# Kernel optimization log

Measured on AMD Instinct MI355X. Metric: run time of the kernel, lower is better.

The kernel has to match this reference:

```python
import jax, jax.numpy as jnp
import numpy as np

POOL_SCALES = (1, 3, 6, 8)
CHANNELS = 256
BN_EPS = 1e-5


def _pool_matrix(in_size, out_size):
    # Row i averages input slots [floor(i*in/out), ceil((i+1)*in/out)) -- matches AdaptiveAvgPool2d.
    P = np.zeros((out_size, in_size), np.float32)
    for i in range(out_size):
        s = (i * in_size) // out_size
        e = -((-(i + 1) * in_size) // out_size)
        P[i, s:e] = 1.0 / (e - s)
    return jnp.asarray(P)


def _bn(x, g, b, m, v):
    # inference-mode BatchNorm2d on NCHW
    inv = g * jax.lax.rsqrt(v + BN_EPS)
    return x * inv[None, :, None, None] + (b - m * inv)[None, :, None, None]


def _conv1x1(x, w):
    # 1x1 conv == channel matmul: w [Cout, Cin], x [B, Cin, H, W]
    return jnp.einsum('oc,bchw->bohw', w, x)


def _ppm_concat(x):
    # x: [B, C, H, W] -> [B, C, sum(s*s)]
    B, C, H, W = x.shape
    outs = []
    for s in POOL_SCALES:
        Ph = _pool_matrix(H, s)
        Pw = _pool_matrix(W, s)
        pooled = jnp.einsum('ih,jw,bchw->bcij', Ph, Pw, x)
        outs.append(pooled.reshape(B, C, -1))
    return jnp.concatenate(outs, axis=2)


def setup_inputs() -> dict:
    key = jax.random.key(0)
    ks = jax.random.split(key, 24)
    B, Cl, Ch, Cmid, Cout, H, W = 8, 1024, 2048, 256, 2048, 64, 64
    return {
        'low_feats': jax.random.normal(ks[0], (B, Cl, H, W), jnp.float32),
        'high_feats': jax.random.normal(ks[1], (B, Ch, H, W), jnp.float32),
        'q_w': jax.random.normal(ks[2], (Cmid, Ch), jnp.float32) * 0.02,
        'q_g': jax.random.uniform(ks[3], (Cmid,), jnp.float32, 0.5, 1.5),
        'q_b': jax.random.normal(ks[4], (Cmid,), jnp.float32) * 0.1,
        'q_m': jax.random.normal(ks[5], (Cmid,), jnp.float32) * 0.1,
        'q_v': jax.random.uniform(ks[6], (Cmid,), jnp.float32, 0.5, 1.5),
        'k_w': jax.random.normal(ks[7], (Cmid, Cl), jnp.float32) * 0.02,
        'k_g': jax.random.uniform(ks[8], (Cmid,), jnp.float32, 0.5, 1.5),
        'k_b': jax.random.normal(ks[9], (Cmid,), jnp.float32) * 0.1,
        'k_m': jax.random.normal(ks[10], (Cmid,), jnp.float32) * 0.1,
        'k_v': jax.random.uniform(ks[11], (Cmid,), jnp.float32, 0.5, 1.5),
        'v_w': jax.random.normal(ks[12], (Cmid, Cl), jnp.float32) * 0.02,
        'v_b': jax.random.normal(ks[13], (Cmid,), jnp.float32) * 0.02,
        'o_w': jax.random.normal(ks[14], (Cout, Cmid), jnp.float32) * 0.02,
        'o_b': jax.random.normal(ks[15], (Cout,), jnp.float32) * 0.02,
        'bn_w': jax.random.normal(ks[16], (Cout, Cout + Ch), jnp.float32) * 0.02,
        'bn_g': jax.random.uniform(ks[17], (Cout,), jnp.float32, 0.5, 1.5),
        'bn_b': jax.random.normal(ks[18], (Cout,), jnp.float32) * 0.1,
        'bn_m': jax.random.normal(ks[19], (Cout,), jnp.float32) * 0.1,
        'bn_v': jax.random.uniform(ks[20], (Cout,), jnp.float32, 0.5, 1.5),
    }


def reference(low_feats, high_feats, q_w, q_g, q_b, q_m, q_v,
              k_w, k_g, k_b, k_m, k_v, v_w, v_b, o_w, o_b,
              bn_w, bn_g, bn_b, bn_m, bn_v):
    B, _, H, W = high_feats.shape
    # query: ConvModule (1x1 conv, BN, ReLU) on high-level feats; query_scale=1 -> no downsample
    q = jax.nn.relu(_bn(_conv1x1(high_feats, q_w), q_g, q_b, q_m, q_v))
    q = q.reshape(B, CHANNELS, H * W).transpose(0, 2, 1)  # [B, N, C]
    # key: ConvModule then pyramid-pooled; value: plain 1x1 conv then pyramid-pooled
    k = jax.nn.relu(_bn(_conv1x1(low_feats, k_w), k_g, k_b, k_m, k_v))
    k = _ppm_concat(k)  # [B, C, M]
    v = _conv1x1(low_feats, v_w) + v_b[None, :, None, None]
    v = _ppm_concat(v).transpose(0, 2, 1)  # [B, M, C]
    # matmul-normalized attention with pooled K/V (M = 110, tiny)
    sim = jnp.einsum('bnc,bcm->bnm', q, k) * (CHANNELS ** -0.5)
    sim = jax.nn.softmax(sim, axis=-1)
    ctx = jnp.einsum('bnm,bmc->bnc', sim, v)  # [B, N, C]
    ctx = ctx.transpose(0, 2, 1).reshape(B, CHANNELS, H, W)
    # out projection: plain 1x1 conv with bias
    ctx = _conv1x1(ctx, o_w) + o_b[None, :, None, None]  # [B, Cout, H, W]
    # single stage (query_scales=(1,)), stack+sum is identity
    # bottleneck: 1x1 conv (no bias) + BN, no activation
    fused = jnp.concatenate([ctx, high_feats], axis=1)
    out = _bn(_conv1x1(fused, bn_w), bn_g, bn_b, bn_m, bn_v)
    return out
```

## Files before the change

### kernel.cpp

```cpp
#include <hip/hip_runtime.h>
#include <hip/hip_bf16.h>

typedef unsigned int u32;
typedef unsigned short u16;
typedef short s16x8 __attribute__((ext_vector_type(8)));
typedef float f32x4 __attribute__((ext_vector_type(4)));
typedef u16 u16x4 __attribute__((ext_vector_type(4)));

__device__ __forceinline__ u16 f2b(float x) {
  u32 u = __float_as_uint(x);
  return (u16)((u + 0x7fffu + ((u >> 16) & 1u)) >> 16);
}
__device__ __forceinline__ float b2f(u16 x) { return __uint_as_float(((u32)x) << 16); }

__device__ __forceinline__ void gload16(const void* g, void* l) {
  __builtin_amdgcn_global_load_lds((const __attribute__((address_space(1))) u32*)g,
                                   (__attribute__((address_space(3))) u32*)l, 16, 0, 0);
}

template <int OUT_BF16>
__global__ __launch_bounds__(512, 2) void gemm256(
    const u16* __restrict__ A, long long sA, int lda,
    const u16* __restrict__ B1, long long sB1, int K1,
    const u16* __restrict__ B2, long long sB2, int K2,
    void* __restrict__ Cv, long long sC, int ldc,
    const float* __restrict__ bias, int bias_mode,
    int relu_limit, float alpha) {
  const int K = K1 + K2, nt = K >> 5;
  const int b = blockIdx.z, tm = blockIdx.x, tn = blockIdx.y;
  const u16* Ab = A + (size_t)b * sA + (size_t)tm * 256 * lda;
  const u16* B1b = B1 + (size_t)b * sB1 + (size_t)tn * 256 * K1;
  const u16* B2b = B2 ? (B2 + (size_t)b * sB2 + (size_t)tn * 256 * K2) : (const u16*)0;

  __shared__ u16 lds[32768];

  const int tt = threadIdx.x, w = tt >> 6, l = tt & 63;
  const int wr = w >> 2, wc = w & 3;

  int sx[2], sdst[2];
#pragma unroll
  for (int i = 0; i < 2; ++i) {
    const int lin = (i * 512 + tt) << 4;
    sx[i] = lin ^ (((lin >> 7) & 7) << 4);
    sdst[i] = (i * 512 + w * 64) << 3;
  }

  auto stage = [&](int kt) {
    const int buf = (kt & 1) << 14;
    const int kk = kt << 5;
#pragma unroll
    for (int i = 0; i < 2; ++i) {
      const int x = sx[i];
      gload16(Ab + (size_t)(x >> 6) * lda + kk + ((x & 63) >> 1), &lds[buf + sdst[i]]);
    }
    const u16* Bb; int ld, kloc;
    if (kk < K1) { Bb = B1b; ld = K1; kloc = kk; }
    else         { Bb = B2b; ld = K2; kloc = kk - K1; }
#pragma unroll
    for (int i = 0; i < 2; ++i) {
      const int x = sx[i];
      gload16(Bb + (size_t)(x >> 6) * ld + kloc + ((x & 63) >> 1), &lds[buf + 8192 + sdst[i]]);
    }
  };

  stage(0);
  stage(1);

  f32x4 acc[8][4] = {};
  const int lr = l & 15, lk16 = (l >> 4) << 4;

  for (int t = 0; t < nt; ++t) {
    const int buf = (t & 1) << 14;
    if (t == nt - 1) asm volatile("s_waitcnt vmcnt(0)" ::: "memory");
    else             asm volatile("s_waitcnt vmcnt(4)" ::: "memory");
    __builtin_amdgcn_s_barrier();

    const char* Abuf = (const char*)&lds[buf];
    const char* Bbuf = (const char*)&lds[buf + 8192];
    s16x8 bfr[4], af[8];
#pragma unroll
    for (int j = 0; j < 4; ++j) {
      const int lin = ((wc * 64 + j * 16 + lr) << 6) | lk16;
      bfr[j] = *reinterpret_cast<const s16x8*>(Bbuf + (lin ^ (((lin >> 7) & 7) << 4)));
    }
#pragma unroll
    for (int m = 0; m < 8; ++m) {
      const int lin = ((wr * 128 + m * 16 + lr) << 6) | lk16;
      af[m] = *reinterpret_cast<const s16x8*>(Abuf + (lin ^ (((lin >> 7) & 7) << 4)));
    }
    __builtin_amdgcn_s_setprio(1);
#pragma unroll
    for (int m = 0; m < 4; ++m)
#pragma unroll
      for (int j = 0; j < 4; ++j)
        acc[m][j] = __builtin_amdgcn_mfma_f32_16x16x32_bf16(af[m], bfr[j], acc[m][j], 0, 0, 0);
    __builtin_amdgcn_s_setprio(0);

    asm volatile("s_waitcnt lgkmcnt(0)" ::: "memory");
    __builtin_amdgcn_s_barrier();
    if (t + 2 < nt) stage(t + 2);

    __builtin_amdgcn_s_setprio(1);
#pragma unroll
    for (int m = 4; m < 8; ++m)
#pragma unroll
      for (int j = 0; j < 4; ++j)
        acc[m][j] = __builtin_amdgcn_mfma_f32_16x16x32_bf16(af[m], bfr[j], acc[m][j], 0, 0, 0);
    __builtin_amdgcn_s_setprio(0);
  }

  const int li = (l >> 4) * 4;
#pragma unroll
  for (int m = 0; m < 8; ++m) {
    const int row = tm * 256 + wr * 128 + m * 16 + li;
#pragma unroll
    for (int j = 0; j < 4; ++j) {
      const int col = tn * 256 + wc * 64 + j * 16 + lr;
      const float bc = (bias_mode == 1) ? bias[col] : 0.f;
#pragma unroll
      for (int i = 0; i < 4; ++i) {
        float v = acc[m][j][i] * alpha;
        v += (bias_mode == 2) ? bias[row + i] : bc;
        if (col < relu_limit) v = fmaxf(v, 0.f);
        const size_t idx = (size_t)b * sC + (size_t)(row + i) * ldc + col;
        if (OUT_BF16) ((u16*)Cv)[idx] = f2b(v);
        else          ((float*)Cv)[idx] = v;
      }
    }
  }
}

template <int OUT_BF16>
__global__ __launch_bounds__(256) void gemm_bt(
    const u16* __restrict__ A, long long sA, int lda,
    const u16* __restrict__ B1, long long sB1, int K1,
    const u16* __restrict__ B2, long long sB2, int K2,
    void* __restrict__ Cv, long long sC, int ldc,
    const float* __restrict__ bias, int bias_mode,
    int relu_limit, float alpha) {
  const int K = K1 + K2;
  const int b = blockIdx.z;
  const int tm = blockIdx.x, tn = blockIdx.y;
  const u16* Ab = A + (size_t)b * sA;
  const u16* B1b = B1 + (size_t)b * sB1;
  const u16* B2b = B2 ? (B2 + (size_t)b * sB2) : (const u16*)0;

  __shared__ u16 As[128 * 32];
  __shared__ u16 Bs[128 * 32];

  const int t = threadIdx.x;
  const int w = t >> 6, l = t & 63;
  const int wr = w >> 1, wc = w & 1;
  const int srow = w * 16 + (l >> 2);
  const int scol = (l & 3) * 8;
  u16* AsW = As + w * 512;
  u16* BsW = Bs + w * 512;

  f32x4 acc[4][4] = {};
  const int lr = l & 15, lk = (l >> 4) * 8;

  for (int kk = 0; kk < K; kk += 32) {
    __syncthreads();
    {
      const u16* g0 = Ab + (size_t)(tm * 128 + srow) * lda + (kk + scol);
      gload16(g0, AsW);
      gload16(g0 + (size_t)64 * lda, AsW + 2048);
    }
    {
      const u16* bb; int ld, kloc;
      if (kk < K1) { bb = B1b; ld = K1; kloc = kk; }
      else         { bb = B2b; ld = K2; kloc = kk - K1; }
      const u16* g0 = bb + (size_t)(tn * 128 + srow) * ld + (kloc + scol);
      gload16(g0, BsW);
      gload16(g0 + (size_t)64 * ld, BsW + 2048);
    }
    __syncthreads();
    s16x8 af[4], bfr[4];
#pragma unroll
    for (int m = 0; m < 4; ++m)
      af[m] = *reinterpret_cast<const s16x8*>(&As[(wr * 64 + m * 16 + lr) * 32 + lk]);
#pragma unroll
    for (int j = 0; j < 4; ++j)
      bfr[j] = *reinterpret_cast<const s16x8*>(&Bs[(wc * 64 + j * 16 + lr) * 32 + lk]);
#pragma unroll
    for (int m = 0; m < 4; ++m)
#pragma unroll
      for (int j = 0; j < 4; ++j)
        acc[m][j] = __builtin_amdgcn_mfma_f32_16x16x32_bf16(af[m], bfr[j], acc[m][j], 0, 0, 0);
  }

  const int li = (l >> 4) * 4;
#pragma unroll
  for (int m = 0; m < 4; ++m) {
    const int row = tm * 128 + wr * 64 + m * 16 + li;
#pragma unroll
    for (int j = 0; j < 4; ++j) {
      const int col = tn * 128 + wc * 64 + j * 16 + lr;
      const float bc = (bias_mode == 1) ? bias[col] : 0.f;
#pragma unroll
      for (int i = 0; i < 4; ++i) {
        float v = acc[m][j][i] * alpha;
        v += (bias_mode == 2) ? bias[row + i] : bc;
        if (col < relu_limit) v = fmaxf(v, 0.f);
        const size_t idx = (size_t)b * sC + (size_t)(row + i) * ldc + col;
        if (OUT_BF16) ((u16*)Cv)[idx] = f2b(v);
        else          ((float*)Cv)[idx] = v;
      }
    }
  }
}

__global__ __launch_bounds__(256) void transpose_cvt(
    const float* __restrict__ in, u16* __restrict__ out, int R, int C) {
  const int b = blockIdx.z;
  in += (size_t)b * R * C;
  out += (size_t)b * R * C;
  const int ct = blockIdx.x, rt = blockIdx.y;
  __shared__ float tile[64][65];
  const int t = threadIdx.x;
  {
    const int c4 = (t & 15) * 4, r0 = t >> 4;
    const float* src = in + (size_t)(rt * 64 + r0) * C + ct * 64 + c4;
#pragma unroll
    for (int i = 0; i < 4; ++i) {
      const float4 v = *reinterpret_cast<const float4*>(src + (size_t)(i * 16) * C);
      tile[r0 + i * 16][c4 + 0] = v.x; tile[r0 + i * 16][c4 + 1] = v.y;
      tile[r0 + i * 16][c4 + 2] = v.z; tile[r0 + i * 16][c4 + 3] = v.w;
    }
  }
  __syncthreads();
  {
    const int r4 = (t & 15) * 4, c0 = t >> 4;
    u16* dst = out + (size_t)(ct * 64 + c0) * R + rt * 64 + r4;
#pragma unroll
    for (int i = 0; i < 4; ++i) {
      u16x4 o;
      o.x = f2b(tile[r4 + 0][c0 + i * 16]);
      o.y = f2b(tile[r4 + 1][c0 + i * 16]);
      o.z = f2b(tile[r4 + 2][c0 + i * 16]);
      o.w = f2b(tile[r4 + 3][c0 + i * 16]);
      *reinterpret_cast<u16x4*>(dst + (size_t)(i * 16) * R) = o;
    }
  }
}

__global__ __launch_bounds__(256) void prep_wq(const float* __restrict__ qw,
    const float* __restrict__ qg, const float* __restrict__ qb_,
    const float* __restrict__ qm, const float* __restrict__ qv,
    u16* __restrict__ Wq, float* __restrict__ qbias) {
  const int i = blockIdx.x * 256 + threadIdx.x;
  const int o = i >> 11, c = i & 2047;
  const float inv = qg[o] * rsqrtf(qv[o] + 1e-5f);
  Wq[i] = f2b(qw[i] * inv);
  if (c == 0) qbias[o] = qb_[o] - qm[o] * inv;
}

__global__ __launch_bounds__(256) void prep_wkv(const float* __restrict__ kw,
    const float* __restrict__ kg, const float* __restrict__ kb,
    const float* __restrict__ km, const float* __restrict__ kv,
    const float* __restrict__ vw, const float* __restrict__ vb,
    u16* __restrict__ Wkv, float* __restrict__ kvbias) {
  const int i = blockIdx.x * 256 + threadIdx.x;
  const int r = i >> 10, c = i & 1023;
  if (r < 256) {
    const float inv = kg[r] * rsqrtf(kv[r] + 1e-5f);
    Wkv[i] = f2b(kw[i] * inv);
    if (c == 0) kvbias[r] = kb[r] - km[r] * inv;
  } else {
    Wkv[i] = f2b(vw[(size_t)(r - 256) * 1024 + c]);
    if (c == 0) kvbias[r] = vb[r - 256];
  }
}

__global__ __launch_bounds__(256) void prep_bn(const float* __restrict__ bn_w,
    const float* __restrict__ g, const float* __restrict__ v_,
    u16* __restrict__ bn1s, u16* __restrict__ Wfin) {
  const int i = blockIdx.x * 256 + threadIdx.x;
  const int o = i >> 11, j = i & 2047;
  const float inv = g[o] * rsqrtf(v_[o] + 1e-5f);
  bn1s[i] = f2b(bn_w[(size_t)o * 4096 + j] * inv);
  Wfin[(size_t)o * 2304 + j] = f2b(bn_w[(size_t)o * 4096 + 2048 + j] * inv);
}

__global__ __launch_bounds__(256) void prep_fbias(const float* __restrict__ bn_w,
    const float* __restrict__ o_b, const float* __restrict__ g,
    const float* __restrict__ bb, const float* __restrict__ m_,
    const float* __restrict__ v_, float* __restrict__ fbias) {
  const int o = blockIdx.x, t = threadIdx.x;
  float s = 0.f;
  for (int j = t; j < 2048; j += 256) s += bn_w[(size_t)o * 4096 + j] * o_b[j];
  for (int off = 32; off; off >>= 1) s += __shfl_xor(s, off);
  __shared__ float red[4];
  if ((t & 63) == 0) red[t >> 6] = s;
  __syncthreads();
  if (t == 0) {
    const float tot = red[0] + red[1] + red[2] + red[3];
    const float inv = g[o] * rsqrtf(v_[o] + 1e-5f);
    fbias[o] = inv * tot + bb[o] - m_[o] * inv;
  }
}

__device__ __forceinline__ void jj_to_range(int jj, int& s, int& j, int& c0, int& c1) {
  if (jj < 1)       { s = 1; j = jj; }
  else if (jj < 4)  { s = 3; j = jj - 1; }
  else if (jj < 10) { s = 6; j = jj - 4; }
  else              { s = 8; j = jj - 10; }
  c0 = (j * 64) / s;
  c1 = ((j + 1) * 64 + s - 1) / s;
}

__global__ __launch_bounds__(256) void pool_cols(const u16* __restrict__ kvT,
                                                 float* __restrict__ cp) {
  const int b = blockIdx.y, r = blockIdx.x, t = threadIdx.x;
  const u16* base = kvT + ((size_t)b * 4096 + (size_t)r * 64) * 512;
  const int ch0 = (t & 63) * 8;
  for (int jj = (t >> 6); jj < 18; jj += 4) {
    int s, j, c0, c1;
    jj_to_range(jj, s, j, c0, c1);
    float acc[8] = {0.f, 0.f, 0.f, 0.f, 0.f, 0.f, 0.f, 0.f};
    for (int c = c0; c < c1; ++c) {
      const s16x8 v = *reinterpret_cast<const s16x8*>(base + (size_t)c * 512 + ch0);
#pragma unroll
      for (int i = 0; i < 8; ++i) acc[i] += b2f((u16)v[i]);
    }
    float* o = cp + (((size_t)(b * 64 + r) * 18 + jj) * 512 + ch0);
    *reinterpret_cast<float4*>(o)     = make_float4(acc[0], acc[1], acc[2], acc[3]);
    *reinterpret_cast<float4*>(o + 4) = make_float4(acc[4], acc[5], acc[6], acc[7]);
  }
}

__global__ __launch_bounds__(256) void pool_rows(const float* __restrict__ cp,
    u16* __restrict__ Kp, u16* __restrict__ Vp) {
  const int b = blockIdx.y, m = blockIdx.x, t = threadIdx.x;
  if (m >= 110) {
    Kp[((size_t)b * 128 + m) * 256 + t] = 0;
    Vp[((size_t)b * 256 + t) * 128 + m] = 0;
    return;
  }
  int s, idx, jjbase;
  if (m < 1)       { s = 1; idx = m;      jjbase = 0; }
  else if (m < 10) { s = 3; idx = m - 1;  jjbase = 1; }
  else if (m < 46) { s = 6; idx = m - 10; jjbase = 4; }
  else             { s = 8; idx = m - 46; jjbase = 10; }
  const int i = idx / s, j = idx % s;
  const int jj = jjbase + j;
  const int r0 = (i * 64) / s, r1 = ((i + 1) * 64 + s - 1) / s;
  const int c0 = (j * 64) / s, c1 = ((j + 1) * 64 + s - 1) / s;
  float a0 = 0.f, a1 = 0.f;
  for (int r = r0; r < r1; ++r) {
    const float* px = cp + ((size_t)(b * 64 + r) * 18 + jj) * 512;
    a0 += px[t];
    a1 += px[t + 256];
  }
  const float inv = 1.f / (float)((r1 - r0) * (c1 - c0));
  Kp[((size_t)b * 128 + m) * 256 + t] = f2b(a0 * inv);
  Vp[((size_t)b * 256 + t) * 128 + m] = f2b(a1 * inv);
}

__global__ __launch_bounds__(256) void softmax_rows(const float* __restrict__ sim,
                                                    u16* __restrict__ P) {
  const int row = blockIdx.x * 4 + (threadIdx.x >> 6);
  const int l = threadIdx.x & 63;
  const float* s = sim + (size_t)row * 128;
  const float v0 = (l < 110) ? s[l] : -1e30f;
  const float v1 = (l + 64 < 110) ? s[l + 64] : -1e30f;
  float mx = fmaxf(v0, v1);
  for (int off = 32; off; off >>= 1) mx = fmaxf(mx, __shfl_xor(mx, off));
  const float e0 = (l < 110) ? __expf(v0 - mx) : 0.f;
  const float e1 = (l + 64 < 110) ? __expf(v1 - mx) : 0.f;
  float sum = e0 + e1;
  for (int off = 32; off; off >>= 1) sum += __shfl_xor(sum, off);
  const float inv = 1.f / sum;
  u16* p = P + (size_t)row * 128;
  p[l] = f2b(e0 * inv);
  p[l + 64] = f2b(e1 * inv);
}

extern "C" void kernel_launch(void* const* d_in, const int* in_sizes, int n_in,
                              void* d_out, int out_size, void* d_ws, size_t ws_size,
                              hipStream_t stream) {
  (void)in_sizes; (void)n_in; (void)out_size; (void)ws_size;
  const float* low  = (const float*)d_in[0];
  const float* high = (const float*)d_in[1];
  const float* q_w = (const float*)d_in[2];
  const float* q_g = (const float*)d_in[3];
  const float* q_b = (const float*)d_in[4];
  const float* q_m = (const float*)d_in[5];
  const float* q_v = (const float*)d_in[6];
  const float* k_w = (const float*)d_in[7];
  const float* k_g = (const float*)d_in[8];
  const float* k_b = (const float*)d_in[9];
  const float* k_m = (const float*)d_in[10];
  const float* k_v = (const float*)d_in[11];
  const float* v_w = (const float*)d_in[12];
  const float* v_b = (const float*)d_in[13];
  const float* o_w = (const float*)d_in[14];
  const float* o_b = (const float*)d_in[15];
  const float* bn_w = (const float*)d_in[16];
  const float* bn_g = (const float*)d_in[17];
  const float* bn_b = (const float*)d_in[18];
  const float* bn_m = (const float*)d_in[19];
  const float* bn_v = (const float*)d_in[20];
  float* out = (float*)d_out;

  char* ws = (char*)d_ws;
  size_t off = 0;
  auto alloc = [&](size_t bytes) -> char* {
    char* p = ws + off;
    off += (bytes + 255) & ~(size_t)255;
    return p;
  };
  u16* XhT  = (u16*)alloc(134217728ull);
  u16* qT   = (u16*)alloc(16777216ull);
  u16* XlT  = (u16*)alloc(67108864ull);
  u16* kvT  = (u16*)alloc(33554432ull);
  u16* ctxT = (u16*)alloc(16777216ull);
  u16* Kpool = (u16*)alloc(524288ull);
  u16* VpT   = (u16*)alloc(524288ull);
  u16* Wq   = (u16*)alloc(1048576ull);
  u16* Wkv  = (u16*)alloc(1048576ull);
  u16* Wfin = (u16*)alloc(9437184ull);
  float* qbias  = (float*)alloc(1024);
  float* kvbias = (float*)alloc(2048);
  float* fbias  = (float*)alloc(8192);
  u16* bn1s = qT;
  u16* owT  = ctxT;
  float* sim = (float*)XlT;
  float* cp  = (float*)((char*)XlT + 25165824ull);
  u16* P = kvT;

  prep_bn<<<16384, 256, 0, stream>>>(bn_w, bn_g, bn_v, bn1s, Wfin);
  prep_fbias<<<2048, 256, 0, stream>>>(bn_w, o_b, bn_g, bn_b, bn_m, bn_v, fbias);
  prep_wq<<<2048, 256, 0, stream>>>(q_w, q_g, q_b, q_m, q_v, Wq, qbias);
  prep_wkv<<<2048, 256, 0, stream>>>(k_w, k_g, k_b, k_m, k_v, v_w, v_b, Wkv, kvbias);
  transpose_cvt<<<dim3(4, 32, 1), 256, 0, stream>>>(o_w, owT, 2048, 256);
  gemm_bt<1><<<dim3(16, 2, 1), 256, 0, stream>>>(
      bn1s, 0, 2048, owT, 0, 2048, (const u16*)0, 0, 0,
      (void*)(Wfin + 2048), 0, 2304, (const float*)0, 0, 0, 1.0f);

  transpose_cvt<<<dim3(64, 32, 8), 256, 0, stream>>>(high, XhT, 2048, 4096);
  transpose_cvt<<<dim3(64, 16, 8), 256, 0, stream>>>(low, XlT, 1024, 4096);

  gemm_bt<1><<<dim3(32, 2, 8), 256, 0, stream>>>(
      XhT, 4096ll * 2048, 2048, Wq, 0, 2048, (const u16*)0, 0, 0,
      qT, 4096ll * 256, 256, qbias, 1, 256, 1.0f);
  gemm256<1><<<dim3(16, 2, 8), 512, 0, stream>>>(
      XlT, 4096ll * 1024, 1024, Wkv, 0, 1024, (const u16*)0, 0, 0,
      kvT, 4096ll * 512, 512, kvbias, 1, 256, 1.0f);
  pool_cols<<<dim3(64, 8), 256, 0, stream>>>(kvT, cp);
  pool_rows<<<dim3(128, 8), 256, 0, stream>>>(cp, Kpool, VpT);
  gemm_bt<0><<<dim3(32, 1, 8), 256, 0, stream>>>(
      qT, 4096ll * 256, 256, Kpool, 128ll * 256, 256, (const u16*)0, 0, 0,
      sim, 4096ll * 128, 128, (const float*)0, 0, 0, 0.0625f);
  softmax_rows<<<8192, 256, 0, stream>>>(sim, P);
  gemm_bt<1><<<dim3(32, 2, 8), 256, 0, stream>>>(
      P, 4096ll * 128, 128, VpT, 256ll * 128, 128, (const u16*)0, 0, 0,
      ctxT, 4096ll * 256, 256, (const float*)0, 0, 0, 1.0f);
  gemm256<0><<<dim3(8, 16, 8), 512, 0, stream>>>(
      Wfin, 0, 2304, XhT, 4096ll * 2048, 2048, ctxT, 4096ll * 256, 256,
      out, 2048ll * 4096, 4096, fbias, 2, 0, 1.0f);
}
```

Baseline: 777.3 us.

## Deepen 256x256 GEMM K-tile to 64 with ping-pong barrier schedule and batch-interleaved block order

The main 256x256 bf16 MFMA GEMM now stages 64-wide K tiles (128 KB LDS double buffer) instead of 32. It splits each tile into four MFMA phases separated by s_barrier, sched_barrier and setprio so LDS reads and global prefetch interleave with matrix work across the two co-resident waves. It also remaps the block index so consecutive blocks walk across batches, which is meant to improve L2 reuse of shared tiles. The aim is fewer barriers per FLOP and better MFMA utilization. The cost is much higher LDS use, which may cut occupancy from the declared 2 blocks per CU, plus many extra barriers.

```diff
diff --git a/kernel.cpp b/kernel.cpp
--- a/kernel.cpp
+++ b/kernel.cpp
@@ -16,6 +16,9 @@
 __device__ __forceinline__ void gload16(const void* g, void* l) {
   __builtin_amdgcn_global_load_lds((const __attribute__((address_space(1))) u32*)g,
                                    (__attribute__((address_space(3))) u32*)l, 16, 0, 0);
+}
+__device__ __forceinline__ f32x4 mfma16(s16x8 a, s16x8 b, f32x4 c) {
+  return __builtin_amdgcn_mfma_f32_16x16x32_bf16(a, b, c, 0, 0, 0);
 }
 
 template <int OUT_BF16>
@@ -26,90 +29,133 @@
     void* __restrict__ Cv, long long sC, int ldc,
     const float* __restrict__ bias, int bias_mode,
     int relu_limit, float alpha) {
-  const int K = K1 + K2, nt = K >> 5;
-  const int b = blockIdx.z, tm = blockIdx.x, tn = blockIdx.y;
+  const int K = K1 + K2, nt = K >> 6;
+  int tm, tn, b;
+  {
+    const int flat = blockIdx.x + gridDim.x * (blockIdx.y + gridDim.y * blockIdx.z);
+    if (gridDim.z == 8) {
+      const int slot = flat >> 3;
+      b = flat & 7;
+      tm = slot % gridDim.x;
+      tn = slot / gridDim.x;
+    } else { tm = blockIdx.x; tn = blockIdx.y; b = blockIdx.z; }
+  }
   const u16* Ab = A + (size_t)b * sA + (size_t)tm * 256 * lda;
   const u16* B1b = B1 + (size_t)b * sB1 + (size_t)tn * 256 * K1;
   const u16* B2b = B2 ? (B2 + (size_t)b * sB2 + (size_t)tn * 256 * K2) : (const u16*)0;
 
-  __shared__ u16 lds[32768];
+  __shared__ __attribute__((aligned(128))) char lds[131072];
 
   const int tt = threadIdx.x, w = tt >> 6, l = tt & 63;
   const int wr = w >> 2, wc = w & 3;
-
-  int sx[2], sdst[2];
-#pragma unroll
-  for (int i = 0; i < 2; ++i) {
-    const int lin = (i * 512 + tt) << 4;
-    sx[i] = lin ^ (((lin >> 7) & 7) << 4);
-    sdst[i] = (i * 512 + w * 64) << 3;
-  }
+  const int lr = l & 15, g16 = l >> 4;
+  const int sxl = (lr & 7) << 4;
 
   auto stage = [&](int kt) {
-    const int buf = (kt & 1) << 14;
-    const int kk = kt << 5;
-#pragma unroll
-    for (int i = 0; i < 2; ++i) {
-      const int x = sx[i];
-      gload16(Ab + (size_t)(x >> 6) * lda + kk + ((x & 63) >> 1), &lds[buf + sdst[i]]);
+    const int bufB = (kt & 1) << 16;
+    const int kk = kt << 6;
+#pragma unroll
+    for (int g = 0; g < 4; ++g) {
+      const int lin = (g << 13) | (tt << 4);
+      const int x = lin ^ (((lin >> 7) & 7) << 4);
+      gload16(Ab + (size_t)(x >> 7) * lda + kk + ((x & 127) >> 1),
+              lds + bufB + (g << 13) + (w << 10));
     }
     const u16* Bb; int ld, kloc;
     if (kk < K1) { Bb = B1b; ld = K1; kloc = kk; }
     else         { Bb = B2b; ld = K2; kloc = kk - K1; }
 #pragma unroll
-    for (int i = 0; i < 2; ++i) {
-      const int x = sx[i];
-      gload16(Bb + (size_t)(x >> 6) * ld + kloc + ((x & 63) >> 1), &lds[buf + 8192 + sdst[i]]);
+    for (int g = 0; g < 4; ++g) {
+      const int lin = (g << 13) | (tt << 4);
+      const int x = lin ^ (((lin >> 7) & 7) << 4);
+      gload16(Bb + (size_t)(x >> 7) * ld + kloc + ((x & 127) >> 1),
+              lds + bufB + 32768 + (g << 13) + (w << 10));
     }
   };
 
   stage(0);
-  stage(1);
+  if (nt > 1) stage(1);
 
   f32x4 acc[8][4] = {};
-  const int lr = l & 15, lk16 = (l >> 4) << 4;
+  s16x8 af[8], bf[4];
 
   for (int t = 0; t < nt; ++t) {
-    const int buf = (t & 1) << 14;
-    if (t == nt - 1) asm volatile("s_waitcnt vmcnt(0)" ::: "memory");
-    else             asm volatile("s_waitcnt vmcnt(4)" ::: "memory");
-    __builtin_amdgcn_s_barrier();
-
-    const char* Abuf = (const char*)&lds[buf];
-    const char* Bbuf = (const char*)&lds[buf + 8192];
-    s16x8 bfr[4], af[8];
-#pragma unroll
-    for (int j = 0; j < 4; ++j) {
-      const int lin = ((wc * 64 + j * 16 + lr) << 6) | lk16;
-      bfr[j] = *reinterpret_cast<const s16x8*>(Bbuf + (lin ^ (((lin >> 7) & 7) << 4)));
-    }
+    const int bufB = (t & 1) << 16;
+    const char* Al = lds + bufB;
+    const char* Bl = lds + bufB + 32768;
+    if (t + 1 < nt) asm volatile("s_waitcnt vmcnt(8)" ::: "memory");
+    else            asm volatile("s_waitcnt vmcnt(0)" ::: "memory");
+    __builtin_amdgcn_s_barrier();
+
+#pragma unroll
+    for (int m = 0; m < 8; ++m)
+      af[m] = *reinterpret_cast<const s16x8*>(
+          Al + ((wr * 128 + m * 16 + lr) << 7) + ((g16 << 4) ^ sxl));
+#pragma unroll
+    for (int n = 0; n < 2; ++n)
+      bf[n] = *reinterpret_cast<const s16x8*>(
+          Bl + ((wc * 64 + n * 16 + lr) << 7) + ((g16 << 4) ^ sxl));
+    __builtin_amdgcn_s_barrier();
+    asm volatile("s_waitcnt lgkmcnt(0)" ::: "memory");
+    __builtin_amdgcn_sched_barrier(0);
+    __builtin_amdgcn_s_setprio(1);
 #pragma unroll
     for (int m = 0; m < 8; ++m) {
-      const int lin = ((wr * 128 + m * 16 + lr) << 6) | lk16;
-      af[m] = *reinterpret_cast<const s16x8*>(Abuf + (lin ^ (((lin >> 7) & 7) << 4)));
-    }
+      acc[m][0] = mfma16(af[m], bf[0], acc[m][0]);
+      acc[m][1] = mfma16(af[m], bf[1], acc[m][1]);
+    }
+    __builtin_amdgcn_s_setprio(0);
+    __builtin_amdgcn_s_barrier();
+
+#pragma unroll
+    for (int n = 2; n < 4; ++n)
+      bf[n] = *reinterpret_cast<const s16x8*>(
+          Bl + ((wc * 64 + n * 16 + lr) << 7) + ((g16 << 4) ^ sxl));
+    __builtin_amdgcn_s_barrier();
+    asm volatile("s_waitcnt lgkmcnt(0)" ::: "memory");
+    __builtin_amdgcn_sched_barrier(0);
     __builtin_amdgcn_s_setprio(1);
 #pragma unroll
-    for (int m = 0; m < 4; ++m)
-#pragma unroll
-      for (int j = 0; j < 4; ++j)
-        acc[m][j] = __builtin_amdgcn_mfma_f32_16x16x32_bf16(af[m], bfr[j], acc[m][j], 0, 0, 0);
+    for (int m = 0; m < 8; ++m) {
+      acc[m][2] = mfma16(af[m], bf[2], acc[m][2]);
+      acc[m][3] = mfma16(af[m], bf[3], acc[m][3]);
+    }
     __builtin_amdgcn_s_setprio(0);
-
+    __builtin_amdgcn_s_barrier();
+
+#pragma unroll
+    for (int m = 0; m < 8; ++m)
+      af[m] = *reinterpret_cast<const s16x8*>(
+          Al + ((wr * 128 + m * 16 + lr) << 7) + ((64 | (g16 << 4)) ^ sxl));
+#pragma unroll
+    for (int n = 0; n < 4; ++n)
+      bf[n] = *reinterpret_cast<const s16x8*>(
+          Bl + ((wc * 64 + n * 16 + lr) << 7) + ((64 | (g16 << 4)) ^ sxl));
+    __builtin_amdgcn_s_barrier();
     asm volatile("s_waitcnt lgkmcnt(0)" ::: "memory");
-    __builtin_amdgcn_s_barrier();
+    __builtin_amdgcn_sched_barrier(0);
+    __builtin_amdgcn_s_setprio(1);
+#pragma unroll
+    for (int m = 0; m < 8; ++m) {
+      acc[m][0] = mfma16(af[m], bf[0], acc[m][0]);
+      acc[m][1] = mfma16(af[m], bf[1], acc[m][1]);
+    }
+    __builtin_amdgcn_s_setprio(0);
+    __builtin_amdgcn_s_barrier();
+
     if (t + 2 < nt) stage(t + 2);
-
+    __builtin_amdgcn_s_barrier();
     __builtin_amdgcn_s_setprio(1);
 #pragma unroll
-    for (int m = 4; m < 8; ++m)
-#pragma unroll
-      for (int j = 0; j < 4; ++j)
-        acc[m][j] = __builtin_amdgcn_mfma_f32_16x16x32_bf16(af[m], bfr[j], acc[m][j], 0, 0, 0);
+    for (int m = 0; m < 8; ++m) {
+      acc[m][2] = mfma16(af[m], bf[2], acc[m][2]);
+      acc[m][3] = mfma16(af[m], bf[3], acc[m][3]);
+    }
     __builtin_amdgcn_s_setprio(0);
-  }
-
-  const int li = (l >> 4) * 4;
+    __builtin_amdgcn_s_barrier();
+  }
+
+  const int li = g16 * 4;
 #pragma unroll
   for (int m = 0; m < 8; ++m) {
     const int row = tm * 256 + wr * 128 + m * 16 + li;
@@ -186,7 +232,7 @@
     for (int m = 0; m < 4; ++m)
 #pragma unroll
       for (int j = 0; j < 4; ++j)
-        acc[m][j] = __builtin_amdgcn_mfma_f32_16x16x32_bf16(af[m], bfr[j], acc[m][j], 0, 0, 0);
+        acc[m][j] = mfma16(af[m], bfr[j], acc[m][j]);
   }
 
   const int li = (l >> 4) * 4;
```

Result: slower. 796.7 us (+2.5%).
